# Performance work log

Hardware: AMD Instinct MI355X
Metric: run time of the kernel (lower is better)

## Reference

```python
import jax, jax.numpy as jnp
import numpy as np

DIM = 1024
HEADS = 16
HEAD_DIM = DIM // HEADS
EPS = 1e-6

def _layernorm(x, gamma, beta):
    # LayerNorm over last axis (head_dim), biased variance like torch
    mu = jnp.mean(x, axis=-1, keepdims=True)
    var = jnp.mean(jnp.square(x - mu), axis=-1, keepdims=True)
    return (x - mu) * jax.lax.rsqrt(var + EPS) * gamma + beta

def setup_inputs() -> dict:
    key = jax.random.key(0)
    ks = jax.random.split(key, 12)
    B, N, D = 2, 2048, DIM
    s = 1.0 / np.sqrt(D)
    inp = {
        'x': jax.random.normal(ks[0], (B, N, D), jnp.float32),
        'attn_bias': jax.random.normal(ks[1], (B, 1, N, N), jnp.float32),
        'Wq': jax.random.normal(ks[2], (D, D), jnp.float32) * s,
        'bq': jnp.zeros((D,), jnp.float32),
        'Wk': jax.random.normal(ks[3], (D, D), jnp.float32) * s,
        'bk': jnp.zeros((D,), jnp.float32),
        'Wv': jax.random.normal(ks[4], (D, D), jnp.float32) * s,
        'bv': jnp.zeros((D,), jnp.float32),
        'Wo': jax.random.normal(ks[5], (D, D), jnp.float32) * s,
        'bo': jnp.zeros((D,), jnp.float32),
        'q_gamma': jnp.ones((HEAD_DIM,), jnp.float32),
        'q_beta': jnp.zeros((HEAD_DIM,), jnp.float32),
        'k_gamma': jnp.ones((HEAD_DIM,), jnp.float32),
        'k_beta': jnp.zeros((HEAD_DIM,), jnp.float32),
    }
    return inp

def reference(x, attn_bias, Wq, bq, Wk, bk, Wv, bv, Wo, bo, q_gamma, q_beta, k_gamma, k_beta):
    B, N, D = x.shape
    h, dh = HEADS, HEAD_DIM
    # QKV projections (torch Linear: x @ W.T + b) -> (B, h, N, dh)
    def proj(W, b):
        y = jnp.einsum('bnd,ed->bne', x, W) + b
        return y.reshape(B, N, h, dh).transpose(0, 2, 1, 3)
    q = proj(Wq, bq)
    k = proj(Wk, bk)
    v = proj(Wv, bv)
    # per-head LayerNorm on Q and K
    q = _layernorm(q, q_gamma, q_beta)
    k = _layernorm(k, k_gamma, k_beta)
    # scaled dot-product attention with additive graph bias
    scores = jnp.einsum('bhnd,bhmd->bhnm', q, k) / np.sqrt(dh).astype(np.float32)
    scores = scores + attn_bias  # (B,1,N,N) broadcasts over heads
    attn = jax.nn.softmax(scores, axis=-1)
    out = jnp.einsum('bhnm,bhmd->bhnd', attn, v)
    out = out.transpose(0, 2, 1, 3).reshape(B, N, D)
    return jnp.einsum('bnd,ed->bne', out, Wo) + bo
```

## Files before the change

### kernel.cpp

```cpp
#include <hip/hip_runtime.h>
#include <hip/hip_bf16.h>

#define D_MODEL 1024
#define N_SEQ   2048
#define N_B     2
#define M_ROWS  (N_B * N_SEQ)

typedef __attribute__((ext_vector_type(8))) short bf16x8;
typedef __attribute__((ext_vector_type(4))) float f32x4;

typedef const __attribute__((address_space(1))) unsigned int gu32_t;
typedef __attribute__((address_space(3))) unsigned int lu32_t;

__device__ __forceinline__ void gload16(const void* g, void* l) {
  __builtin_amdgcn_global_load_lds((gu32_t*)g, (lu32_t*)l, 16, 0, 0);
}

__device__ inline unsigned short f2bf(float f) {
  union { float f; unsigned int u; } v; v.f = f;
  unsigned int r = (v.u + 0x7FFFu + ((v.u >> 16) & 1u)) >> 16;
  return (unsigned short)r;
}

__device__ __forceinline__ int lds_off(int row, int col ) {
  return row * 64 + (((col >> 3) ^ (row & 7)) << 3) + (col & 7);
}

template<int ROWS>
__device__ __forceinline__ void stage_tile(const unsigned short* gbase, size_t gstride,
                                           unsigned short* lds, int tid) {
  const int wave = tid >> 6;
#pragma unroll
  for (int rnd = 0; rnd < ROWS / 32; ++rnd) {
    int c = rnd * 256 + tid;
    int row = c >> 3, pc = c & 7;
    int gcol = ((pc ^ (row & 7)) << 3);
    gload16(gbase + (size_t)row * gstride + gcol,
            lds + (size_t)(rnd * 256 + wave * 64) * 8);
  }
}

constexpr size_t XEL = (size_t)M_ROWS * D_MODEL;
constexpr size_t WEL = (size_t)D_MODEL * D_MODEL;

__launch_bounds__(256)
__global__ void cvt_kernel(const float* __restrict__ x,
                           const float* __restrict__ wq, const float* __restrict__ wk,
                           const float* __restrict__ wv, const float* __restrict__ wo,
                           unsigned short* __restrict__ dst) {
  size_t i = ((size_t)blockIdx.x * 256 + threadIdx.x) * 8;
  if (i >= XEL + 4 * WEL) return;
  const float* s; size_t off = i;
  if (off < XEL)                { s = x; }
  else if (off < XEL + WEL)     { s = wq; off -= XEL; }
  else if (off < XEL + 2*WEL)   { s = wk; off -= XEL + WEL; }
  else if (off < XEL + 3*WEL)   { s = wv; off -= XEL + 2*WEL; }
  else                          { s = wo; off -= XEL + 3*WEL; }
  float4 f0 = *(const float4*)(s + off);
  float4 f1 = *(const float4*)(s + off + 4);
  unsigned short t[8] = { f2bf(f0.x), f2bf(f0.y), f2bf(f0.z), f2bf(f0.w),
                          f2bf(f1.x), f2bf(f1.y), f2bf(f1.z), f2bf(f1.w) };
  *(uint4*)(dst + i) = *(const uint4*)t;
}

__device__ __forceinline__ void mainloop128(const unsigned short* __restrict__ A,
                                            const unsigned short* __restrict__ Bw,
                                            int m0, int e0,
                                            unsigned short* As, unsigned short* Bs,
                                            f32x4 (&acc)[4][4]) {
  const int tid  = threadIdx.x;
  const int wave = tid >> 6, lane = tid & 63;
  const int l16 = lane & 15, quad = lane >> 4;
  const int wr = wave >> 1, wc = wave & 1;

  for (int kt = 0; kt < D_MODEL / 64; ++kt) {
    const int k0 = kt * 64;
    stage_tile<128>(A + (size_t)m0 * D_MODEL + k0, D_MODEL, As, tid);
    stage_tile<128>(Bw + (size_t)e0 * D_MODEL + k0, D_MODEL, Bs, tid);
    __syncthreads();
#pragma unroll
    for (int ks = 0; ks < 2; ++ks) {
      bf16x8 af[4], bfr[4];
#pragma unroll
      for (int mi = 0; mi < 4; ++mi)
        af[mi] = *(const bf16x8*)(As + lds_off(wr * 64 + mi * 16 + l16, ks * 32 + quad * 8));
#pragma unroll
      for (int ci = 0; ci < 4; ++ci)
        bfr[ci] = *(const bf16x8*)(Bs + lds_off(wc * 64 + ci * 16 + l16, ks * 32 + quad * 8));
#pragma unroll
      for (int mi = 0; mi < 4; ++mi)
#pragma unroll
        for (int ci = 0; ci < 4; ++ci)
          acc[mi][ci] = __builtin_amdgcn_mfma_f32_16x16x32_bf16(af[mi], bfr[ci], acc[mi][ci], 0, 0, 0);
    }
    __syncthreads();
  }
}

__launch_bounds__(256)
__global__ void qkv_gemm(const unsigned short* __restrict__ xb,
                         const unsigned short* __restrict__ wb,
                         const float* __restrict__ bq, const float* __restrict__ bk,
                         const float* __restrict__ bv,
                         const float* __restrict__ qg, const float* __restrict__ qbeta,
                         const float* __restrict__ kg, const float* __restrict__ kbeta,
                         unsigned short* __restrict__ qkout,
                         unsigned short* __restrict__ vt) {
  __shared__ unsigned short As[128 * 64];
  __shared__ unsigned short Bs[128 * 64];
  const int m0  = blockIdx.x * 128;
  const int by  = blockIdx.y;
  const int mat = by >> 3;
  const int e0  = (by & 7) * 128;
  const unsigned short* Bw = wb + (size_t)mat * WEL;

  f32x4 acc[4][4];
#pragma unroll
  for (int mi = 0; mi < 4; ++mi)
#pragma unroll
    for (int ci = 0; ci < 4; ++ci) acc[mi][ci] = f32x4{0.f, 0.f, 0.f, 0.f};

  mainloop128(xb, Bw, m0, e0, As, Bs, acc);

  const int lane = threadIdx.x & 63, wave = threadIdx.x >> 6;
  const int l16 = lane & 15, quad = lane >> 4;
  const int wr = wave >> 1, wc = wave & 1;
  const int colbase = e0 + wc * 64;

  const float* bias = (mat == 0) ? bq : ((mat == 1) ? bk : bv);
  float bcol[4];
#pragma unroll
  for (int ci = 0; ci < 4; ++ci) bcol[ci] = bias[colbase + ci * 16 + l16];
#pragma unroll
  for (int mi = 0; mi < 4; ++mi)
#pragma unroll
    for (int ci = 0; ci < 4; ++ci)
#pragma unroll
      for (int r = 0; r < 4; ++r) acc[mi][ci][r] += bcol[ci];

  if (mat < 2) {
    const float* gamma = (mat == 0) ? qg : kg;
    const float* beta  = (mat == 0) ? qbeta : kbeta;
    const float sc = (mat == 0) ? 0.125f : 1.0f;
    float g4[4], bt4[4];
#pragma unroll
    for (int ci = 0; ci < 4; ++ci) {
      g4[ci] = gamma[ci * 16 + l16] * sc;
      bt4[ci] = beta[ci * 16 + l16] * sc;
    }
#pragma unroll
    for (int mi = 0; mi < 4; ++mi)
#pragma unroll
      for (int r = 0; r < 4; ++r) {
        float s = acc[mi][0][r] + acc[mi][1][r] + acc[mi][2][r] + acc[mi][3][r];
        s += __shfl_xor(s, 1); s += __shfl_xor(s, 2);
        s += __shfl_xor(s, 4); s += __shfl_xor(s, 8);
        float mean = s * (1.f / 64.f);
        float d0 = acc[mi][0][r] - mean, d1 = acc[mi][1][r] - mean;
        float d2 = acc[mi][2][r] - mean, d3 = acc[mi][3][r] - mean;
        float q = d0 * d0 + d1 * d1 + d2 * d2 + d3 * d3;
        q += __shfl_xor(q, 1); q += __shfl_xor(q, 2);
        q += __shfl_xor(q, 4); q += __shfl_xor(q, 8);
        float rs = rsqrtf(q * (1.f / 64.f) + 1e-6f);
        acc[mi][0][r] = d0 * rs * g4[0] + bt4[0];
        acc[mi][1][r] = d1 * rs * g4[1] + bt4[1];
        acc[mi][2][r] = d2 * rs * g4[2] + bt4[2];
        acc[mi][3][r] = d3 * rs * g4[3] + bt4[3];
      }
    unsigned short* out = qkout + (size_t)mat * XEL;
#pragma unroll
    for (int mi = 0; mi < 4; ++mi)
#pragma unroll
      for (int ci = 0; ci < 4; ++ci) {
        int col = colbase + ci * 16 + l16;
#pragma unroll
        for (int r = 0; r < 4; ++r) {
          int row = m0 + wr * 64 + mi * 16 + quad * 4 + r;
          out[(size_t)row * D_MODEL + col] = f2bf(acc[mi][ci][r]);
        }
      }
  } else {
    unsigned short* scr = ((wave < 2) ? As : Bs) + (size_t)(wave & 1) * 4096;
#pragma unroll
    for (int ci = 0; ci < 4; ++ci) {
      int dl = ci * 16 + l16;
      int sw = (dl & 3) * 16;
#pragma unroll
      for (int mi = 0; mi < 4; ++mi)
#pragma unroll
        for (int r = 0; r < 4; ++r) {
          int nl = mi * 16 + quad * 4 + r;
          scr[dl * 64 + (nl ^ sw)] = f2bf(acc[mi][ci][r]);
        }
    }
    __builtin_amdgcn_wave_barrier();
    int row0 = m0 + wr * 64;
    int b = row0 >> 11, nb = row0 & 2047;
    int h = colbase >> 6;
    int dl = lane;
    unsigned short* gdst = vt + ((size_t)((b * 16 + h) * 64 + dl) * N_SEQ + nb);
    const unsigned short* srow = scr + dl * 64;
    int sw = (dl & 3) * 16;
#pragma unroll
    for (int j = 0; j < 8; ++j) {
      uint4 vv = *(const uint4*)(srow + ((j * 8) ^ sw));
      *(uint4*)(gdst + j * 8) = vv;
    }
  }
}

__launch_bounds__(256)
__global__ void out_gemm(const unsigned short* __restrict__ ao,
                         const unsigned short* __restrict__ wob,
                         const float* __restrict__ bo,
                         float* __restrict__ out) {
  __shared__ unsigned short As[128 * 64];
  __shared__ unsigned short Bs[128 * 64];
  const int m0 = blockIdx.x * 128;
  const int e0 = blockIdx.y * 128;

  f32x4 acc[4][4];
#pragma unroll
  for (int mi = 0; mi < 4; ++mi)
#pragma unroll
    for (int ci = 0; ci < 4; ++ci) acc[mi][ci] = f32x4{0.f, 0.f, 0.f, 0.f};

  mainloop128(ao, wob, m0, e0, As, Bs, acc);

  const int lane = threadIdx.x & 63, wave = threadIdx.x >> 6;
  const int l16 = lane & 15, quad = lane >> 4;
  const int wr = wave >> 1, wc = wave & 1;
  float bcol[4];
#pragma unroll
  for (int ci = 0; ci < 4; ++ci) bcol[ci] = bo[e0 + wc * 64 + ci * 16 + l16];
#pragma unroll
  for (int mi = 0; mi < 4; ++mi)
#pragma unroll
    for (int ci = 0; ci < 4; ++ci) {
      int col = e0 + wc * 64 + ci * 16 + l16;
#pragma unroll
      for (int r = 0; r < 4; ++r) {
        int row = m0 + wr * 64 + mi * 16 + quad * 4 + r;
        out[(size_t)row * D_MODEL + col] = acc[mi][ci][r] + bcol[ci];
      }
    }
}

__launch_bounds__(256)
__global__ void attn_kernel(const unsigned short* __restrict__ Q,
                            const unsigned short* __restrict__ Kn,
                            const unsigned short* __restrict__ Vt,
                            const float* __restrict__ bias,
                            unsigned short* __restrict__ Out) {
  __shared__ unsigned short Qs[128 * 64];
  __shared__ unsigned short Ks[2][64 * 64];
  __shared__ unsigned short Vts[2][64 * 64];
  const int tid  = threadIdx.x;
  const int wave = tid >> 6, lane = tid & 63;
  const int quad = lane >> 4, l16 = lane & 15;
  const int bidx = blockIdx.x;
  const int qt = bidx & 15;
  const int h  = (bidx >> 4) & 15;
  const int b  = bidx >> 8;
  const int q0 = qt * 128;
  const size_t base  = (size_t)b * N_SEQ * D_MODEL + (size_t)h * 64;
  const unsigned short* vtb = Vt + (size_t)(b * 16 + h) * 64 * N_SEQ;

  stage_tile<128>(Q + base + (size_t)q0 * D_MODEL, D_MODEL, Qs, tid);
  stage_tile<64>(Kn + base, D_MODEL, Ks[0], tid);
  stage_tile<64>(vtb, N_SEQ, Vts[0], tid);
  __syncthreads();
  bf16x8 aq[2][2];
#pragma unroll
  for (int mi = 0; mi < 2; ++mi)
#pragma unroll
    for (int ks = 0; ks < 2; ++ks)
      aq[mi][ks] = *(const bf16x8*)(Qs + lds_off(wave * 32 + mi * 16 + l16, ks * 32 + quad * 8));
  __builtin_amdgcn_wave_barrier();

  f32x4 o[2][4];
#pragma unroll
  for (int mi = 0; mi < 2; ++mi)
#pragma unroll
    for (int c = 0; c < 4; ++c) o[mi][c] = f32x4{0.f, 0.f, 0.f, 0.f};
  float lrow[2][4] = {{0.f,0.f,0.f,0.f},{0.f,0.f,0.f,0.f}};

  constexpr int NT = N_SEQ / 64;
  for (int kt = 0; kt < NT; ++kt) {
    const int cur = kt & 1;
    if (kt + 1 < NT) {
      stage_tile<64>(Kn + base + (size_t)(kt + 1) * 64 * D_MODEL, D_MODEL, Ks[cur ^ 1], tid);
      stage_tile<64>(vtb + (kt + 1) * 64, N_SEQ, Vts[cur ^ 1], tid);
    }

    const float* bptr = bias + ((size_t)b * N_SEQ + q0 + wave * 32 + quad * 4) * N_SEQ + kt * 64;
    float breg[2][4][4];
#pragma unroll
    for (int mi = 0; mi < 2; ++mi)
#pragma unroll
      for (int c = 0; c < 4; ++c)
#pragma unroll
        for (int r = 0; r < 4; ++r)
          breg[mi][c][r] = bptr[(size_t)(mi * 16 + r) * N_SEQ + c * 16 + l16];

    f32x4 sf[2][4];
#pragma unroll
    for (int c = 0; c < 4; ++c) {
      bf16x8 b0 = *(const bf16x8*)(Ks[cur] + lds_off(c * 16 + l16, quad * 8));
      bf16x8 b1 = *(const bf16x8*)(Ks[cur] + lds_off(c * 16 + l16, 32 + quad * 8));
#pragma unroll
      for (int mi = 0; mi < 2; ++mi) {
        f32x4 z = f32x4{0.f, 0.f, 0.f, 0.f};
        z = __builtin_amdgcn_mfma_f32_16x16x32_bf16(aq[mi][0], b0, z, 0, 0, 0);
        sf[mi][c] = __builtin_amdgcn_mfma_f32_16x16x32_bf16(aq[mi][1], b1, z, 0, 0, 0);
      }
    }

    __builtin_amdgcn_wave_barrier();
#pragma unroll
    for (int mi = 0; mi < 2; ++mi)
#pragma unroll
      for (int c = 0; c < 4; ++c)
#pragma unroll
        for (int r = 0; r < 4; ++r) {
          float p = __expf(sf[mi][c][r] + breg[mi][c][r]);
          lrow[mi][r] += p;
          Qs[lds_off(wave * 32 + mi * 16 + quad * 4 + r, c * 16 + l16)] = f2bf(p);
        }
    __builtin_amdgcn_wave_barrier();

#pragma unroll
    for (int ks = 0; ks < 2; ++ks) {
      bf16x8 bv[4];
#pragma unroll
      for (int c = 0; c < 4; ++c)
        bv[c] = *(const bf16x8*)(Vts[cur] + lds_off(c * 16 + l16, ks * 32 + quad * 8));
#pragma unroll
      for (int mi = 0; mi < 2; ++mi) {
        bf16x8 pa = *(const bf16x8*)(Qs + lds_off(wave * 32 + mi * 16 + l16, ks * 32 + quad * 8));
#pragma unroll
        for (int c = 0; c < 4; ++c)
          o[mi][c] = __builtin_amdgcn_mfma_f32_16x16x32_bf16(pa, bv[c], o[mi][c], 0, 0, 0);
      }
    }
    __syncthreads();
  }

#pragma unroll
  for (int mi = 0; mi < 2; ++mi)
#pragma unroll
    for (int r = 0; r < 4; ++r) {
      float l = lrow[mi][r];
      l += __shfl_xor(l, 1); l += __shfl_xor(l, 2);
      l += __shfl_xor(l, 4); l += __shfl_xor(l, 8);
      float inv = 1.0f / l;
      size_t row = (size_t)b * N_SEQ + q0 + wave * 32 + mi * 16 + quad * 4 + r;
#pragma unroll
      for (int c = 0; c < 4; ++c)
        Out[row * D_MODEL + h * 64 + c * 16 + l16] = f2bf(o[mi][c][r] * inv);
    }
}

extern "C" void kernel_launch(void* const* d_in, const int* in_sizes, int n_in,
                              void* d_out, int out_size, void* d_ws, size_t ws_size,
                              hipStream_t stream) {
  const float* x    = (const float*)d_in[0];
  const float* bias = (const float*)d_in[1];
  const float* Wq = (const float*)d_in[2];  const float* bq = (const float*)d_in[3];
  const float* Wk = (const float*)d_in[4];  const float* bk = (const float*)d_in[5];
  const float* Wv = (const float*)d_in[6];  const float* bv = (const float*)d_in[7];
  const float* Wo = (const float*)d_in[8];  const float* bo = (const float*)d_in[9];
  const float* qg = (const float*)d_in[10]; const float* qb = (const float*)d_in[11];
  const float* kg = (const float*)d_in[12]; const float* kb = (const float*)d_in[13];
  float* out = (float*)d_out;

  unsigned short* wsb = (unsigned short*)d_ws;
  unsigned short* xb  = wsb;
  unsigned short* wqb = wsb + XEL;
  unsigned short* wob = wsb + XEL + 3 * WEL;
  unsigned short* qn  = wsb + XEL + 4 * WEL;
  unsigned short* kn  = qn + XEL;
  unsigned short* vt  = qn + 2 * XEL;
  unsigned short* ao  = xb;

  dim3 blk(256, 1, 1);

  cvt_kernel<<<dim3((unsigned)((XEL + 4 * WEL) / (256 * 8)), 1, 1), blk, 0, stream>>>(
      x, Wq, Wk, Wv, Wo, wsb);

  qkv_gemm<<<dim3(M_ROWS / 128, 24, 1), blk, 0, stream>>>(
      xb, wqb, bq, bk, bv, qg, qb, kg, kb, qn, vt);

  attn_kernel<<<dim3(N_B * 16 * (N_SEQ / 128), 1, 1), blk, 0, stream>>>(qn, kn, vt, bias, ao);

  out_gemm<<<dim3(M_ROWS / 128, D_MODEL / 128, 1), blk, 0, stream>>>(ao, wob, bo, out);
}
```

Before: 278.6 us.

## Transpose attention MFMA layout so P stays in registers, prefetch bias vectors

Swaps the MFMA operand order so scores come out transposed (key rows per lane), which lets the exponentiated probabilities be packed directly into bf16 A-operands in registers instead of round-tripping through shared memory. The V-transpose scratch ordering is permuted to match. Bias is now loaded as f32x4 vectors and prefetched one tile ahead, and exp uses exp2 with log2e folded into the Q scale. This removes LDS writes and reads plus wave barriers per tile, at the cost of extra registers for double-buffered bias.

Result: faster. 263.3 us (-5.5%).

```diff
diff --git a/kernel.cpp b/kernel.cpp
--- a/kernel.cpp
+++ b/kernel.cpp
@@ -20,6 +20,20 @@
   union { float f; unsigned int u; } v; v.f = f;
   unsigned int r = (v.u + 0x7FFFu + ((v.u >> 16) & 1u)) >> 16;
   return (unsigned short)r;
+}
+
+__device__ __forceinline__ unsigned int cvt_pk_bf16(float a, float b) {
+  unsigned int r;
+  asm("v_cvt_pk_bf16_f32 %0, %1, %2" : "=v"(r) : "v"(a), "v"(b));
+  return r;
+}
+
+__device__ __forceinline__ float exp2fast(float x) {
+#if __has_builtin(__builtin_amdgcn_exp2f)
+  return __builtin_amdgcn_exp2f(x);
+#else
+  return __expf(x * 0.69314718056f);
+#endif
 }
 
 __device__ __forceinline__ int lds_off(int row, int col ) {
@@ -141,7 +155,7 @@
   if (mat < 2) {
     const float* gamma = (mat == 0) ? qg : kg;
     const float* beta  = (mat == 0) ? qbeta : kbeta;
-    const float sc = (mat == 0) ? 0.125f : 1.0f;
+    const float sc = (mat == 0) ? 0.18033688011112042f : 1.0f;
     float g4[4], bt4[4];
 #pragma unroll
     for (int ci = 0; ci < 4; ++ci) {
@@ -189,8 +203,8 @@
       for (int mi = 0; mi < 4; ++mi)
 #pragma unroll
         for (int r = 0; r < 4; ++r) {
-          int nl = mi * 16 + quad * 4 + r;
-          scr[dl * 64 + (nl ^ sw)] = f2bf(acc[mi][ci][r]);
+          int np = ((mi >> 1) << 5) + (quad << 3) + ((mi & 1) << 2) + r;
+          scr[dl * 64 + (np ^ sw)] = f2bf(acc[mi][ci][r]);
         }
     }
     __builtin_amdgcn_wave_barrier();
@@ -269,6 +283,19 @@
   stage_tile<128>(Q + base + (size_t)q0 * D_MODEL, D_MODEL, Qs, tid);
   stage_tile<64>(Kn + base, D_MODEL, Ks[0], tid);
   stage_tile<64>(vtb, N_SEQ, Vts[0], tid);
+
+  const float* brow[2];
+#pragma unroll
+  for (int mi = 0; mi < 2; ++mi)
+    brow[mi] = bias + ((size_t)b * N_SEQ + q0 + wave * 32 + mi * 16 + l16) * N_SEQ;
+
+  f32x4 bcur[2][4], bnxt[2][4];
+#pragma unroll
+  for (int mi = 0; mi < 2; ++mi)
+#pragma unroll
+    for (int c = 0; c < 4; ++c)
+      bcur[mi][c] = *(const f32x4*)(brow[mi] + c * 16 + quad * 4);
+
   __syncthreads();
   bf16x8 aq[2][2];
 #pragma unroll
@@ -276,14 +303,14 @@
 #pragma unroll
     for (int ks = 0; ks < 2; ++ks)
       aq[mi][ks] = *(const bf16x8*)(Qs + lds_off(wave * 32 + mi * 16 + l16, ks * 32 + quad * 8));
-  __builtin_amdgcn_wave_barrier();
 
   f32x4 o[2][4];
 #pragma unroll
   for (int mi = 0; mi < 2; ++mi)
 #pragma unroll
-    for (int c = 0; c < 4; ++c) o[mi][c] = f32x4{0.f, 0.f, 0.f, 0.f};
-  float lrow[2][4] = {{0.f,0.f,0.f,0.f},{0.f,0.f,0.f,0.f}};
+    for (int cd = 0; cd < 4; ++cd) o[mi][cd] = f32x4{0.f, 0.f, 0.f, 0.f};
+  float lsum[2] = {0.f, 0.f};
+  constexpr float LOG2E = 1.44269504088896340736f;
 
   constexpr int NT = N_SEQ / 64;
   for (int kt = 0; kt < NT; ++kt) {
@@ -291,74 +318,75 @@
     if (kt + 1 < NT) {
       stage_tile<64>(Kn + base + (size_t)(kt + 1) * 64 * D_MODEL, D_MODEL, Ks[cur ^ 1], tid);
       stage_tile<64>(vtb + (kt + 1) * 64, N_SEQ, Vts[cur ^ 1], tid);
-    }
-
-    const float* bptr = bias + ((size_t)b * N_SEQ + q0 + wave * 32 + quad * 4) * N_SEQ + kt * 64;
-    float breg[2][4][4];
-#pragma unroll
-    for (int mi = 0; mi < 2; ++mi)
-#pragma unroll
-      for (int c = 0; c < 4; ++c)
-#pragma unroll
-        for (int r = 0; r < 4; ++r)
-          breg[mi][c][r] = bptr[(size_t)(mi * 16 + r) * N_SEQ + c * 16 + l16];
-
-    f32x4 sf[2][4];
+#pragma unroll
+      for (int mi = 0; mi < 2; ++mi)
+#pragma unroll
+        for (int c = 0; c < 4; ++c)
+          bnxt[mi][c] = *(const f32x4*)(brow[mi] + (kt + 1) * 64 + c * 16 + quad * 4);
+    }
+
+    f32x4 sfT[2][4];
 #pragma unroll
     for (int c = 0; c < 4; ++c) {
-      bf16x8 b0 = *(const bf16x8*)(Ks[cur] + lds_off(c * 16 + l16, quad * 8));
-      bf16x8 b1 = *(const bf16x8*)(Ks[cur] + lds_off(c * 16 + l16, 32 + quad * 8));
+      bf16x8 k0 = *(const bf16x8*)(Ks[cur] + lds_off(c * 16 + l16, quad * 8));
+      bf16x8 k1 = *(const bf16x8*)(Ks[cur] + lds_off(c * 16 + l16, 32 + quad * 8));
 #pragma unroll
       for (int mi = 0; mi < 2; ++mi) {
         f32x4 z = f32x4{0.f, 0.f, 0.f, 0.f};
-        z = __builtin_amdgcn_mfma_f32_16x16x32_bf16(aq[mi][0], b0, z, 0, 0, 0);
-        sf[mi][c] = __builtin_amdgcn_mfma_f32_16x16x32_bf16(aq[mi][1], b1, z, 0, 0, 0);
+        z = __builtin_amdgcn_mfma_f32_16x16x32_bf16(k0, aq[mi][0], z, 0, 0, 0);
+        sfT[mi][c] = __builtin_amdgcn_mfma_f32_16x16x32_bf16(k1, aq[mi][1], z, 0, 0, 0);
       }
     }
 
-    __builtin_amdgcn_wave_barrier();
+    union PafU { unsigned int w[4]; bf16x8 v; };
+    PafU paf[2][2];
 #pragma unroll
     for (int mi = 0; mi < 2; ++mi)
 #pragma unroll
-      for (int c = 0; c < 4; ++c)
-#pragma unroll
-        for (int r = 0; r < 4; ++r) {
-          float p = __expf(sf[mi][c][r] + breg[mi][c][r]);
-          lrow[mi][r] += p;
-          Qs[lds_off(wave * 32 + mi * 16 + quad * 4 + r, c * 16 + l16)] = f2bf(p);
-        }
-    __builtin_amdgcn_wave_barrier();
+      for (int c = 0; c < 4; ++c) {
+        float p0 = exp2fast(fmaf(bcur[mi][c][0], LOG2E, sfT[mi][c][0]));
+        float p1 = exp2fast(fmaf(bcur[mi][c][1], LOG2E, sfT[mi][c][1]));
+        float p2 = exp2fast(fmaf(bcur[mi][c][2], LOG2E, sfT[mi][c][2]));
+        float p3 = exp2fast(fmaf(bcur[mi][c][3], LOG2E, sfT[mi][c][3]));
+        lsum[mi] += (p0 + p1) + (p2 + p3);
+        paf[mi][c >> 1].w[(c & 1) * 2]     = cvt_pk_bf16(p0, p1);
+        paf[mi][c >> 1].w[(c & 1) * 2 + 1] = cvt_pk_bf16(p2, p3);
+      }
 
 #pragma unroll
     for (int ks = 0; ks < 2; ++ks) {
       bf16x8 bv[4];
 #pragma unroll
-      for (int c = 0; c < 4; ++c)
-        bv[c] = *(const bf16x8*)(Vts[cur] + lds_off(c * 16 + l16, ks * 32 + quad * 8));
-#pragma unroll
-      for (int mi = 0; mi < 2; ++mi) {
-        bf16x8 pa = *(const bf16x8*)(Qs + lds_off(wave * 32 + mi * 16 + l16, ks * 32 + quad * 8));
-#pragma unroll
-        for (int c = 0; c < 4; ++c)
-          o[mi][c] = __builtin_amdgcn_mfma_f32_16x16x32_bf16(pa, bv[c], o[mi][c], 0, 0, 0);
-      }
+      for (int cd = 0; cd < 4; ++cd)
+        bv[cd] = *(const bf16x8*)(Vts[cur] + lds_off(cd * 16 + l16, ks * 32 + quad * 8));
+#pragma unroll
+      for (int mi = 0; mi < 2; ++mi)
+#pragma unroll
+        for (int cd = 0; cd < 4; ++cd)
+          o[mi][cd] = __builtin_amdgcn_mfma_f32_16x16x32_bf16(bv[cd], paf[mi][ks].v, o[mi][cd], 0, 0, 0);
     }
     __syncthreads();
+#pragma unroll
+    for (int mi = 0; mi < 2; ++mi)
+#pragma unroll
+      for (int c = 0; c < 4; ++c) bcur[mi][c] = bnxt[mi][c];
   }
 
 #pragma unroll
-  for (int mi = 0; mi < 2; ++mi)
-#pragma unroll
-    for (int r = 0; r < 4; ++r) {
-      float l = lrow[mi][r];
-      l += __shfl_xor(l, 1); l += __shfl_xor(l, 2);
-      l += __shfl_xor(l, 4); l += __shfl_xor(l, 8);
-      float inv = 1.0f / l;
-      size_t row = (size_t)b * N_SEQ + q0 + wave * 32 + mi * 16 + quad * 4 + r;
-#pragma unroll
-      for (int c = 0; c < 4; ++c)
-        Out[row * D_MODEL + h * 64 + c * 16 + l16] = f2bf(o[mi][c][r] * inv);
-    }
+  for (int mi = 0; mi < 2; ++mi) {
+    float l = lsum[mi];
+    l += __shfl_xor(l, 16);
+    l += __shfl_xor(l, 32);
+    float inv = 1.0f / l;
+    size_t row = (size_t)b * N_SEQ + q0 + wave * 32 + mi * 16 + l16;
+#pragma unroll
+    for (int cd = 0; cd < 4; ++cd) {
+      uint2 vv;
+      vv.x = cvt_pk_bf16(o[mi][cd][0] * inv, o[mi][cd][1] * inv);
+      vv.y = cvt_pk_bf16(o[mi][cd][2] * inv, o[mi][cd][3] * inv);
+      *(uint2*)(Out + row * D_MODEL + h * 64 + cd * 16 + quad * 4) = vv;
+    }
+  }
 }
 
 extern "C" void kernel_launch(void* const* d_in, const int* in_sizes, int n_in,
```
